# Performance work log

Hardware: AMD Instinct MI355X
Metric: run time of the kernel (lower is better)

## Reference

```python
import jax, jax.numpy as jnp
import numpy as np

B, S, E = 1, 2048, 4096
HQ, HKV = 32, 8
D = E // HQ          # 128
RATIO = HQ // HKV    # 4
CACHE = 1024
T = CACHE + S        # 3072


def setup_inputs() -> dict:
    key = jax.random.key(0)
    ks = jax.random.split(key, 8)
    sc = lambda fan_in: 1.0 / np.sqrt(fan_in)
    x = jax.random.normal(ks[0], (B, S, E), dtype=jnp.float32)
    w_q = jax.random.normal(ks[1], (E, E), dtype=jnp.float32) * sc(E)
    w_k = jax.random.normal(ks[2], (E, HKV * D), dtype=jnp.float32) * sc(E)
    w_v = jax.random.normal(ks[3], (E, HKV * D), dtype=jnp.float32) * sc(E)
    w_o = jax.random.normal(ks[4], (E, E), dtype=jnp.float32) * sc(E)
    k_cache = jax.random.normal(ks[5], (B, HKV, CACHE, D), dtype=jnp.float32)
    v_cache = jax.random.normal(ks[6], (B, HKV, CACHE, D), dtype=jnp.float32)
    # causal additive mask with cache offset: query i may attend key j iff j <= i + CACHE
    q_pos = jnp.arange(S)[:, None] + CACHE
    k_pos = jnp.arange(T)[None, :]
    attention_mask = jnp.where(k_pos <= q_pos, 0.0, -1e9).astype(jnp.float32)
    return {"x": x, "w_q": w_q, "w_k": w_k, "w_v": w_v, "w_o": w_o,
            "k_cache": k_cache, "v_cache": v_cache, "attention_mask": attention_mask}


def reference(x, w_q, w_k, w_v, w_o, k_cache, v_cache, attention_mask):
    # Projections, split into heads: [B, H, S, D]
    Q = (x @ w_q).reshape(B, S, HQ, D).transpose(0, 2, 1, 3)
    K_new = (x @ w_k).reshape(B, S, HKV, D).transpose(0, 2, 1, 3)
    V_new = (x @ w_v).reshape(B, S, HKV, D).transpose(0, 2, 1, 3)
    # KV-cache concat along time
    K = jnp.concatenate([k_cache, K_new], axis=2)  # [B, HKV, T, D]
    V = jnp.concatenate([v_cache, V_new], axis=2)
    # GQA grouping as in source: (head group) with group = HKV
    Qg = Q.reshape(B, RATIO, HKV, S, D)            # [B, h, g, S, D]
    scores = jnp.einsum('bhgsd,bgtd->bhgst', Qg, K) / jnp.sqrt(jnp.asarray(D, x.dtype))
    scores = scores + attention_mask               # broadcast [S, T]
    att = jax.nn.softmax(scores, axis=-1)
    res = jnp.einsum('bhgst,bgtd->bhgsd', att, V)  # [B, h, g, S, D]
    # '... head group s dhead -> ... s (head group dhead)'
    res = res.transpose(0, 3, 1, 2, 4).reshape(B, S, E)
    out = res @ w_o
    return (out, (K, V))
```

## Files before the change

kernel.cpp:

```cpp
#include <hip/hip_runtime.h>

typedef unsigned short u16;
typedef unsigned int u32;
typedef __attribute__((ext_vector_type(8))) short short8;
typedef __attribute__((ext_vector_type(4))) float f32x4;

#define S_LEN 2048
#define E_DIM 4096
#define NHQ 32
#define NHKV 8
#define HD 128
#define CACHE_LEN 1024
#define T_LEN 3072
#define KV_ELEMS ((size_t)NHKV * T_LEN * HD)

__device__ __forceinline__ u16 f2bf(float f) {
  union { float f; u32 u; } v; v.f = f;
  u32 u = v.u;
  return (u16)((u + 0x7FFFu + ((u >> 16) & 1u)) >> 16);
}

__device__ __forceinline__ void gl_lds16(const void* g, void* l) {
  __builtin_amdgcn_global_load_lds(
      (const __attribute__((address_space(1))) unsigned int*)g,
      (__attribute__((address_space(3))) unsigned int*)l, 16, 0, 0);
}

__global__ __launch_bounds__(256) void cvt_x(const float* __restrict__ x,
                                             u16* __restrict__ xb) {
  int i = blockIdx.x * 256 + threadIdx.x;
  float4 v = ((const float4*)x)[i];
  uint2 o;
  o.x = (u32)f2bf(v.x) | ((u32)f2bf(v.y) << 16);
  o.y = (u32)f2bf(v.z) | ((u32)f2bf(v.w) << 16);
  ((uint2*)xb)[i] = o;
}

__global__ __launch_bounds__(256) void copy_caches(
    const float4* __restrict__ kc, const float4* __restrict__ vc,
    float4* __restrict__ Ko, float4* __restrict__ Vo,
    uint2* __restrict__ Kb) {
  int i = blockIdx.x * 256 + threadIdx.x;
  int h = i >> 15;
  size_t o = (size_t)i + ((size_t)h << 16);
  float4 v = kc[i];
  Ko[o] = v;
  uint2 b;
  b.x = (u32)f2bf(v.x) | ((u32)f2bf(v.y) << 16);
  b.y = (u32)f2bf(v.z) | ((u32)f2bf(v.w) << 16);
  Kb[o] = b;
  Vo[o] = vc[i];
}

__global__ __launch_bounds__(256) void cvt_vcT(const float* __restrict__ vc,
                                               u16* __restrict__ vbT) {
  __shared__ u16 t[64][68];
  const int tid = threadIdx.x;
  const int h = blockIdx.z;
  const int t0 = blockIdx.x << 6;
  const int d0 = blockIdx.y << 6;
  const float* in = vc + ((size_t)h * CACHE_LEN + t0) * HD + d0;
  const int rl = tid >> 4;
  const int c4 = (tid & 15) << 2;
#pragma unroll
  for (int i = 0; i < 4; ++i) {
    int rr = rl + (i << 4);
    float4 v = *(const float4*)&in[(size_t)rr * HD + c4];
    t[c4 + 0][rr] = f2bf(v.x);
    t[c4 + 1][rr] = f2bf(v.y);
    t[c4 + 2][rr] = f2bf(v.z);
    t[c4 + 3][rr] = f2bf(v.w);
  }
  __syncthreads();
  u16* outp = vbT + ((size_t)h * HD + d0) * T_LEN + t0;
#pragma unroll
  for (int p = 0; p < 2; ++p) {
    int idx = tid + (p << 8);
    int dr = idx >> 3;
    int ch = (idx & 7) << 3;
    u32 a0 = (u32)t[dr][ch + 0] | ((u32)t[dr][ch + 1] << 16);
    u32 a1 = (u32)t[dr][ch + 2] | ((u32)t[dr][ch + 3] << 16);
    u32 a2 = (u32)t[dr][ch + 4] | ((u32)t[dr][ch + 5] << 16);
    u32 a3 = (u32)t[dr][ch + 6] | ((u32)t[dr][ch + 7] << 16);
    uint4 o4; o4.x = a0; o4.y = a1; o4.z = a2; o4.w = a3;
    *(uint4*)&outp[(size_t)dr * T_LEN + ch] = o4;
  }
}

__global__ __launch_bounds__(256) void cvt_wt(const float* __restrict__ w,
                                              u16* __restrict__ wt,
                                              int K, int N) {
  __shared__ u16 t[64][68];
  const int tid = threadIdx.x;
  const int ntk = K >> 6;
  const int k0 = (blockIdx.x % ntk) << 6;
  const int n0 = (blockIdx.x / ntk) << 6;
  const int kl = tid >> 4;
  const int nl4 = (tid & 15) << 2;
#pragma unroll
  for (int i = 0; i < 4; ++i) {
    int kk = kl + (i << 4);
    float4 v = *(const float4*)&w[(size_t)(k0 + kk) * N + n0 + nl4];
    t[nl4 + 0][kk] = f2bf(v.x);
    t[nl4 + 1][kk] = f2bf(v.y);
    t[nl4 + 2][kk] = f2bf(v.z);
    t[nl4 + 3][kk] = f2bf(v.w);
  }
  __syncthreads();
  const int onl = tid >> 3;
  const int okc = (tid & 7) << 3;
#pragma unroll
  for (int p = 0; p < 2; ++p) {
    int nl = onl + (p << 5);
    u32 a0 = (u32)t[nl][okc + 0] | ((u32)t[nl][okc + 1] << 16);
    u32 a1 = (u32)t[nl][okc + 2] | ((u32)t[nl][okc + 3] << 16);
    u32 a2 = (u32)t[nl][okc + 4] | ((u32)t[nl][okc + 5] << 16);
    u32 a3 = (u32)t[nl][okc + 6] | ((u32)t[nl][okc + 7] << 16);
    uint4 o4; o4.x = a0; o4.y = a1; o4.z = a2; o4.w = a3;
    *(uint4*)&wt[(size_t)(n0 + nl) * K + k0 + okc] = o4;
  }
}

template<int MODE>
__global__ __launch_bounds__(256) void gemm2(
    const u16* __restrict__ A, const u16* __restrict__ Bt,
    int M, int N, int K,
    float* __restrict__ outF, u16* __restrict__ outB, u16* __restrict__ outB2) {
  __shared__ __align__(16) u16 Als[128 * 32];
  __shared__ __align__(16) u16 Bls[128 * 32];
  const int tid = threadIdx.x;
  const int lane = tid & 63;
  const int wave = tid >> 6;
  const int wr = wave >> 1, wc = wave & 1;
  const int l15 = lane & 15, l4 = lane >> 4;
  const int nbn = N >> 7;
  const int bm0 = (blockIdx.x / nbn) << 7;
  const int bn0 = (blockIdx.x % nbn) << 7;

  f32x4 acc[4][4];
#pragma unroll
  for (int i = 0; i < 4; ++i)
#pragma unroll
    for (int j = 0; j < 4; ++j) {
      acc[i][j][0] = 0.f; acc[i][j][1] = 0.f;
      acc[i][j][2] = 0.f; acc[i][j][3] = 0.f;
    }

  const u16* Abase = A + (size_t)bm0 * K;
  const u16* Bbase = Bt + (size_t)bn0 * K;
  const int c0 = tid, c1 = tid + 256;
  const int r0 = c0 >> 2, q0c = (c0 & 3) << 3;
  const int r1 = c1 >> 2, q1c = (c1 & 3) << 3;

  for (int k0 = 0; k0 < K; k0 += 32) {
    __syncthreads();
    gl_lds16(Abase + (size_t)r0 * K + k0 + q0c, &Als[c0 << 3]);
    gl_lds16(Bbase + (size_t)r0 * K + k0 + q0c, &Bls[c0 << 3]);
    gl_lds16(Abase + (size_t)r1 * K + k0 + q1c, &Als[c1 << 3]);
    gl_lds16(Bbase + (size_t)r1 * K + k0 + q1c, &Bls[c1 << 3]);
    __syncthreads();

    short8 af[4], bfr[4];
#pragma unroll
    for (int mi = 0; mi < 4; ++mi)
      af[mi] = *(const short8*)&Als[((wr << 6) + (mi << 4) + l15) * 32 + (l4 << 3)];
#pragma unroll
    for (int ni = 0; ni < 4; ++ni)
      bfr[ni] = *(const short8*)&Bls[((wc << 6) + (ni << 4) + l15) * 32 + (l4 << 3)];
#pragma unroll
    for (int mi = 0; mi < 4; ++mi)
#pragma unroll
      for (int ni = 0; ni < 4; ++ni)
        acc[mi][ni] = __builtin_amdgcn_mfma_f32_16x16x32_bf16(af[mi], bfr[ni],
                                                              acc[mi][ni], 0, 0, 0);
  }
#pragma unroll
  for (int mi = 0; mi < 4; ++mi) {
#pragma unroll
    for (int ni = 0; ni < 4; ++ni) {
#pragma unroll
      for (int r = 0; r < 4; ++r) {
        int row = bm0 + (wr << 6) + (mi << 4) + (l4 << 2) + r;
        int col = bn0 + (wc << 6) + (ni << 4) + l15;
        float v = acc[mi][ni][r];
        if (MODE == 0) {
          outB[(size_t)row * N + col] = f2bf(v);
        } else if (MODE == 1) {
          int hv = col >> 7;
          int d = col & 127;
          int h = hv & 7;
          if (hv < 8) {
            size_t idx = ((size_t)h * T_LEN + (CACHE_LEN + row)) * HD + d;
            outF[idx] = v;
            outB[idx] = f2bf(v);
          } else {
            size_t idxF = ((size_t)h * T_LEN + (CACHE_LEN + row)) * HD + d + KV_ELEMS;
            outF[idxF] = v;
            outB2[((size_t)h * HD + d) * T_LEN + (CACHE_LEN + row)] = f2bf(v);
          }
        } else {
          outF[(size_t)row * N + col] = v;
        }
      }
    }
  }
}

__global__ __launch_bounds__(256) void attn_fwd(
    const u16* __restrict__ Qb, const u16* __restrict__ Kb,
    const u16* __restrict__ VbT, u16* __restrict__ resB) {
  __shared__ __align__(16) u16 Kls[2][64 * 128];
  __shared__ __align__(16) u16 Vls[2][128 * 64];
  __shared__ __align__(16) u16 Pls[4][16][72];
  const int tid = threadIdx.x;
  const int lane = tid & 63;
  const int wave = tid >> 6;
  const int l15 = lane & 15, l4 = lane >> 4;
  const int hq = blockIdx.y;
  const int kvh = hq & 7;
  const int bx = (hq & 1) ? (31 - (int)blockIdx.x) : (int)blockIdx.x;
  const int q0 = bx << 6;
  const int qw = q0 + (wave << 4);

  short8 aq[4];
  const u16* qrow = Qb + (size_t)(qw + l15) * E_DIM + hq * HD;
#pragma unroll
  for (int kd = 0; kd < 4; ++kd)
    aq[kd] = *(const short8*)(qrow + (kd << 5) + (l4 << 3));

  f32x4 accO[8];
  float mrow[4], lrow[4];
#pragma unroll
  for (int nd = 0; nd < 8; ++nd) {
    accO[nd][0] = 0.f; accO[nd][1] = 0.f; accO[nd][2] = 0.f; accO[nd][3] = 0.f;
  }
#pragma unroll
  for (int r = 0; r < 4; ++r) { mrow[r] = -1e30f; lrow[r] = 0.f; }

  const u16* Kh = Kb + (size_t)kvh * T_LEN * HD;
  const u16* VTh = VbT + (size_t)kvh * (size_t)HD * T_LEN;
  const int nt = bx + 17;

#define STAGE_TILE(T0, BUF)                                                   \
  {                                                                           \
    _Pragma("unroll")                                                         \
    for (int s = 0; s < 4; ++s) {                                             \
      int tr = (wave << 4) + (s << 2) + (lane >> 4);                          \
      int jd = (lane & 15) ^ (tr & 7);                                        \
      gl_lds16(Kh + (size_t)((T0) + tr) * HD + (jd << 3),                     \
               &Kls[BUF][((wave << 2) + s) << 9]);                            \
      int dr = (wave << 5) + (s << 3) + (lane >> 3);                          \
      int tj = (lane & 7) ^ (dr & 7);                                         \
      gl_lds16(VTh + (size_t)dr * T_LEN + (T0) + (tj << 3),                   \
               &Vls[BUF][((wave << 2) + s) << 9]);                            \
    }                                                                         \
  }

  STAGE_TILE(0, 0);
  __syncthreads();

  const float scale = 0.08838834764831845f;
  const int xr = (l15 & 7) << 3;

  for (int it = 0; it < nt; ++it) {
    const int cur = it & 1;
    const int t0 = it << 6;
    if (it + 1 < nt) STAGE_TILE(t0 + 64, cur ^ 1);

    const u16* Kc = &Kls[cur][0];
    const u16* Vc = &Vls[cur][0];

    float p[4][4];
#pragma unroll
    for (int ct = 0; ct < 4; ++ct) {
      f32x4 sc;
      sc[0] = 0.f; sc[1] = 0.f; sc[2] = 0.f; sc[3] = 0.f;
#pragma unroll
      for (int kd = 0; kd < 4; ++kd) {
        short8 bk = *(const short8*)&Kc[((ct << 4) + l15) * 128 +
                                        (((kd << 5) + (l4 << 3)) ^ xr)];
        sc = __builtin_amdgcn_mfma_f32_16x16x32_bf16(aq[kd], bk, sc, 0, 0, 0);
      }
#pragma unroll
      for (int r = 0; r < 4; ++r) p[ct][r] = sc[r] * scale;
    }

    const bool need_mask = (t0 + 63) > (q0 + CACHE_LEN);
    if (need_mask) {
#pragma unroll
      for (int ct = 0; ct < 4; ++ct)
#pragma unroll
        for (int r = 0; r < 4; ++r) {
          int qq = qw + (l4 << 2) + r + CACHE_LEN;
          if (t0 + (ct << 4) + l15 > qq) p[ct][r] = -1e30f;
        }
    }

#pragma unroll
    for (int r = 0; r < 4; ++r) {
      float mx = fmaxf(fmaxf(p[0][r], p[1][r]), fmaxf(p[2][r], p[3][r]));
      mx = fmaxf(mx, __shfl_xor(mx, 1));
      mx = fmaxf(mx, __shfl_xor(mx, 2));
      mx = fmaxf(mx, __shfl_xor(mx, 4));
      mx = fmaxf(mx, __shfl_xor(mx, 8));
      float mn = fmaxf(mrow[r], mx);
      float corr = __expf(mrow[r] - mn);
      mrow[r] = mn;
      float rs = 0.f;
#pragma unroll
      for (int ct = 0; ct < 4; ++ct) {
        p[ct][r] = __expf(p[ct][r] - mn);
        rs += p[ct][r];
      }
      rs += __shfl_xor(rs, 1);
      rs += __shfl_xor(rs, 2);
      rs += __shfl_xor(rs, 4);
      rs += __shfl_xor(rs, 8);
      lrow[r] = lrow[r] * corr + rs;
#pragma unroll
      for (int nd = 0; nd < 8; ++nd) accO[nd][r] *= corr;
    }

#pragma unroll
    for (int ct = 0; ct < 4; ++ct)
#pragma unroll
      for (int r = 0; r < 4; ++r)
        Pls[wave][(l4 << 2) + r][(ct << 4) + l15] = f2bf(p[ct][r]);
    short8 pa0 = *(const short8*)&Pls[wave][l15][l4 << 3];
    short8 pa1 = *(const short8*)&Pls[wave][l15][32 + (l4 << 3)];

#pragma unroll
    for (int nd = 0; nd < 8; ++nd) {
      short8 bv0 = *(const short8*)&Vc[((nd << 4) + l15) * 64 + ((l4 << 3) ^ xr)];
      accO[nd] = __builtin_amdgcn_mfma_f32_16x16x32_bf16(pa0, bv0, accO[nd], 0, 0, 0);
      short8 bv1 = *(const short8*)&Vc[((nd << 4) + l15) * 64 + ((32 + (l4 << 3)) ^ xr)];
      accO[nd] = __builtin_amdgcn_mfma_f32_16x16x32_bf16(pa1, bv1, accO[nd], 0, 0, 0);
    }
    __syncthreads();
  }
#undef STAGE_TILE

#pragma unroll
  for (int nd = 0; nd < 8; ++nd) {
#pragma unroll
    for (int r = 0; r < 4; ++r) {
      float v = accO[nd][r] / lrow[r];
      int q = qw + (l4 << 2) + r;
      int d = (nd << 4) + l15;
      resB[(size_t)q * E_DIM + hq * HD + d] = f2bf(v);
    }
  }
}

extern "C" void kernel_launch(void* const* d_in, const int* in_sizes, int n_in,
                              void* d_out, int out_size, void* d_ws, size_t ws_size,
                              hipStream_t stream) {
  const float* x = (const float*)d_in[0];
  const float* w_q = (const float*)d_in[1];
  const float* w_k = (const float*)d_in[2];
  const float* w_v = (const float*)d_in[3];
  const float* w_o = (const float*)d_in[4];
  const float* k_cache = (const float*)d_in[5];
  const float* v_cache = (const float*)d_in[6];

  float* out = (float*)d_out;
  float* Kout = out + (size_t)S_LEN * E_DIM;

  char* ws = (char*)d_ws;
  const size_t MB = 1024 * 1024;
  u16* xb   = (u16*)(ws);
  u16* resB = (u16*)(ws);
  u16* Qb   = (u16*)(ws + 16 * MB);
  u16* Kb   = (u16*)(ws + 32 * MB);
  u16* VbT  = (u16*)(ws + 38 * MB);
  u16* wkvt = (u16*)(ws + 48 * MB);
  u16* wbig = (u16*)(ws + 64 * MB);

  cvt_x<<<dim3(8192), dim3(256), 0, stream>>>(x, xb);
  copy_caches<<<dim3(1024), dim3(256), 0, stream>>>(
      (const float4*)k_cache, (const float4*)v_cache,
      (float4*)Kout, (float4*)(Kout + KV_ELEMS), (uint2*)Kb);
  cvt_vcT<<<dim3(16, 2, 8), dim3(256), 0, stream>>>(v_cache, VbT);
  cvt_wt<<<dim3(1024), dim3(256), 0, stream>>>(w_k, wkvt, E_DIM, NHKV * HD);
  cvt_wt<<<dim3(1024), dim3(256), 0, stream>>>(w_v, wkvt + (size_t)1024 * E_DIM, E_DIM, NHKV * HD);
  cvt_wt<<<dim3(4096), dim3(256), 0, stream>>>(w_q, wbig, E_DIM, E_DIM);
  gemm2<1><<<dim3(16 * 16), dim3(256), 0, stream>>>(xb, wkvt, S_LEN, 2048, E_DIM, Kout, Kb, VbT);
  gemm2<0><<<dim3(16 * 32), dim3(256), 0, stream>>>(xb, wbig, S_LEN, E_DIM, E_DIM, nullptr, Qb, nullptr);
  cvt_wt<<<dim3(4096), dim3(256), 0, stream>>>(w_o, wbig, E_DIM, E_DIM);
  attn_fwd<<<dim3(32, 32), dim3(256), 0, stream>>>(Qb, Kb, VbT, resB);
  gemm2<2><<<dim3(16 * 32), dim3(256), 0, stream>>>(resB, wbig, S_LEN, E_DIM, E_DIM, out, nullptr, nullptr);
}
```

Measured before the change: 793.2 us.

## Enlarge attention query tile to 256 rows with two row groups per wave

The attention kernel now launches 512-thread blocks that each cover 256 query rows, with every wave processing two 16-row groups. Each staged K/V tile is therefore reused by four times as many queries, cutting global and LDS staging traffic per query. It also adds a lazy softmax rescale that only corrects the accumulators when the row max grows by more than 8, and uses a reciprocal in the epilogue. The costs are higher register pressure, coarser causal tiles that do some extra masked work, and a different block ordering that drops the previous load-balancing flip. The lazy rescale may also change numerics slightly.

```diff
diff --git a/kernel.cpp b/kernel.cpp
--- a/kernel.cpp
+++ b/kernel.cpp
@@ -206,57 +206,69 @@
   }
 }
 
-__global__ __launch_bounds__(256) void attn_fwd(
+__global__ __launch_bounds__(512, 2) void attn_fwd(
     const u16* __restrict__ Qb, const u16* __restrict__ Kb,
     const u16* __restrict__ VbT, u16* __restrict__ resB) {
   __shared__ __align__(16) u16 Kls[2][64 * 128];
   __shared__ __align__(16) u16 Vls[2][128 * 64];
-  __shared__ __align__(16) u16 Pls[4][16][72];
+  __shared__ __align__(16) u16 Pls[8][16][72];
   const int tid = threadIdx.x;
   const int lane = tid & 63;
   const int wave = tid >> 6;
   const int l15 = lane & 15, l4 = lane >> 4;
-  const int hq = blockIdx.y;
+  const int bid = blockIdx.x;
+  const int hq = bid & 31;
+  const int bx = bid >> 5;
   const int kvh = hq & 7;
-  const int bx = (hq & 1) ? (31 - (int)blockIdx.x) : (int)blockIdx.x;
-  const int q0 = bx << 6;
-  const int qw = q0 + (wave << 4);
-
-  short8 aq[4];
-  const u16* qrow = Qb + (size_t)(qw + l15) * E_DIM + hq * HD;
-#pragma unroll
-  for (int kd = 0; kd < 4; ++kd)
-    aq[kd] = *(const short8*)(qrow + (kd << 5) + (l4 << 3));
-
-  f32x4 accO[8];
-  float mrow[4], lrow[4];
-#pragma unroll
-  for (int nd = 0; nd < 8; ++nd) {
-    accO[nd][0] = 0.f; accO[nd][1] = 0.f; accO[nd][2] = 0.f; accO[nd][3] = 0.f;
-  }
-#pragma unroll
-  for (int r = 0; r < 4; ++r) { mrow[r] = -1e30f; lrow[r] = 0.f; }
+  const int q0 = bx << 8;
+  const int qw = q0 + (wave << 5);
+
+  short8 aq[2][4];
+#pragma unroll
+  for (int rg = 0; rg < 2; ++rg) {
+    const u16* qrow = Qb + (size_t)(qw + (rg << 4) + l15) * E_DIM + hq * HD;
+#pragma unroll
+    for (int kd = 0; kd < 4; ++kd)
+      aq[rg][kd] = *(const short8*)(qrow + (kd << 5) + (l4 << 3));
+  }
+
+  f32x4 accO[2][8];
+  float mrow[2][4], lrow[2][4];
+#pragma unroll
+  for (int rg = 0; rg < 2; ++rg) {
+#pragma unroll
+    for (int nd = 0; nd < 8; ++nd) {
+      accO[rg][nd][0] = 0.f; accO[rg][nd][1] = 0.f;
+      accO[rg][nd][2] = 0.f; accO[rg][nd][3] = 0.f;
+    }
+#pragma unroll
+    for (int r = 0; r < 4; ++r) { mrow[rg][r] = -1e30f; lrow[rg][r] = 0.f; }
+  }
 
   const u16* Kh = Kb + (size_t)kvh * T_LEN * HD;
   const u16* VTh = VbT + (size_t)kvh * (size_t)HD * T_LEN;
-  const int nt = bx + 17;
-
-#define STAGE_TILE(T0, BUF)                                                   \
-  {                                                                           \
-    _Pragma("unroll")                                                         \
-    for (int s = 0; s < 4; ++s) {                                             \
-      int tr = (wave << 4) + (s << 2) + (lane >> 4);                          \
-      int jd = (lane & 15) ^ (tr & 7);                                        \
-      gl_lds16(Kh + (size_t)((T0) + tr) * HD + (jd << 3),                     \
-               &Kls[BUF][((wave << 2) + s) << 9]);                            \
-      int dr = (wave << 5) + (s << 3) + (lane >> 3);                          \
-      int tj = (lane & 7) ^ (dr & 7);                                         \
-      gl_lds16(VTh + (size_t)dr * T_LEN + (T0) + (tj << 3),                   \
-               &Vls[BUF][((wave << 2) + s) << 9]);                            \
-    }                                                                         \
-  }
-
-  STAGE_TILE(0, 0);
+  const int nt = (bx << 2) + 20;
+
+  const int trk = (wave << 3) + (lane >> 4);
+  const int jd0 = (lane & 15) ^ (trk & 7);
+  const int jd1 = (lane & 15) ^ ((trk + 4) & 7);
+  const u16* kp0 = Kh + (size_t)trk * HD + (jd0 << 3);
+  const u16* kp1 = Kh + (size_t)(trk + 4) * HD + (jd1 << 3);
+  const int drv = (wave << 4) + (lane >> 3);
+  const int tj0 = (lane & 7) ^ (drv & 7);
+  const u16* vp0 = VTh + (size_t)drv * T_LEN + (tj0 << 3);
+  const u16* vp1 = VTh + (size_t)(drv + 8) * T_LEN + (tj0 << 3);
+
+#define STAGE(BUF)                                             \
+  {                                                            \
+    gl_lds16(kp0, &Kls[BUF][((wave << 1) + 0) << 9]);          \
+    gl_lds16(kp1, &Kls[BUF][((wave << 1) + 1) << 9]);          \
+    gl_lds16(vp0, &Vls[BUF][((wave << 1) + 0) << 9]);          \
+    gl_lds16(vp1, &Vls[BUF][((wave << 1) + 1) << 9]);          \
+    kp0 += 64 * HD; kp1 += 64 * HD; vp0 += 64; vp1 += 64;      \
+  }
+
+  STAGE(0);
   __syncthreads();
 
   const float scale = 0.08838834764831845f;
@@ -265,89 +277,112 @@
   for (int it = 0; it < nt; ++it) {
     const int cur = it & 1;
     const int t0 = it << 6;
-    if (it + 1 < nt) STAGE_TILE(t0 + 64, cur ^ 1);
+    if (it + 1 < nt) STAGE(cur ^ 1);
 
     const u16* Kc = &Kls[cur][0];
     const u16* Vc = &Vls[cur][0];
 
-    float p[4][4];
-#pragma unroll
-    for (int ct = 0; ct < 4; ++ct) {
-      f32x4 sc;
-      sc[0] = 0.f; sc[1] = 0.f; sc[2] = 0.f; sc[3] = 0.f;
-#pragma unroll
-      for (int kd = 0; kd < 4; ++kd) {
-        short8 bk = *(const short8*)&Kc[((ct << 4) + l15) * 128 +
-                                        (((kd << 5) + (l4 << 3)) ^ xr)];
-        sc = __builtin_amdgcn_mfma_f32_16x16x32_bf16(aq[kd], bk, sc, 0, 0, 0);
-      }
-#pragma unroll
-      for (int r = 0; r < 4; ++r) p[ct][r] = sc[r] * scale;
-    }
-
-    const bool need_mask = (t0 + 63) > (q0 + CACHE_LEN);
-    if (need_mask) {
+#pragma unroll
+    for (int rg = 0; rg < 2; ++rg) {
+      const int qrg = qw + (rg << 4);
+      float p[4][4];
+#pragma unroll
+      for (int ct = 0; ct < 4; ++ct) {
+        f32x4 sc;
+        sc[0] = 0.f; sc[1] = 0.f; sc[2] = 0.f; sc[3] = 0.f;
+#pragma unroll
+        for (int kd = 0; kd < 4; ++kd) {
+          short8 bk = *(const short8*)&Kc[((ct << 4) + l15) * 128 +
+                                          (((kd << 5) + (l4 << 3)) ^ xr)];
+          sc = __builtin_amdgcn_mfma_f32_16x16x32_bf16(aq[rg][kd], bk, sc, 0, 0, 0);
+        }
+#pragma unroll
+        for (int r = 0; r < 4; ++r) p[ct][r] = sc[r] * scale;
+      }
+
+      if ((t0 + 63) > (qrg + CACHE_LEN)) {
+#pragma unroll
+        for (int ct = 0; ct < 4; ++ct)
+#pragma unroll
+          for (int r = 0; r < 4; ++r) {
+            int qq = qrg + (l4 << 2) + r + CACHE_LEN;
+            if (t0 + (ct << 4) + l15 > qq) p[ct][r] = -1e30f;
+          }
+      }
+
+      float mx[4];
+#pragma unroll
+      for (int r = 0; r < 4; ++r) {
+        float m = fmaxf(fmaxf(p[0][r], p[1][r]), fmaxf(p[2][r], p[3][r]));
+        m = fmaxf(m, __shfl_xor(m, 1));
+        m = fmaxf(m, __shfl_xor(m, 2));
+        m = fmaxf(m, __shfl_xor(m, 4));
+        m = fmaxf(m, __shfl_xor(m, 8));
+        mx[r] = m;
+      }
+      bool grow = false;
+#pragma unroll
+      for (int r = 0; r < 4; ++r) grow = grow || (mx[r] > mrow[rg][r] + 8.f);
+      if (__any(grow)) {
+#pragma unroll
+        for (int r = 0; r < 4; ++r) {
+          float mn = fmaxf(mrow[rg][r], mx[r]);
+          float corr = __expf(mrow[rg][r] - mn);
+          mrow[rg][r] = mn;
+          lrow[rg][r] *= corr;
+#pragma unroll
+          for (int nd = 0; nd < 8; ++nd) accO[rg][nd][r] *= corr;
+        }
+      }
+#pragma unroll
+      for (int r = 0; r < 4; ++r) {
+        float rs = 0.f;
+#pragma unroll
+        for (int ct = 0; ct < 4; ++ct) {
+          p[ct][r] = __expf(p[ct][r] - mrow[rg][r]);
+          rs += p[ct][r];
+        }
+        rs += __shfl_xor(rs, 1);
+        rs += __shfl_xor(rs, 2);
+        rs += __shfl_xor(rs, 4);
+        rs += __shfl_xor(rs, 8);
+        lrow[rg][r] += rs;
+      }
+
 #pragma unroll
       for (int ct = 0; ct < 4; ++ct)
 #pragma unroll
-        for (int r = 0; r < 4; ++r) {
-          int qq = qw + (l4 << 2) + r + CACHE_LEN;
-          if (t0 + (ct << 4) + l15 > qq) p[ct][r] = -1e30f;
-        }
-    }
-
-#pragma unroll
-    for (int r = 0; r < 4; ++r) {
-      float mx = fmaxf(fmaxf(p[0][r], p[1][r]), fmaxf(p[2][r], p[3][r]));
-      mx = fmaxf(mx, __shfl_xor(mx, 1));
-      mx = fmaxf(mx, __shfl_xor(mx, 2));
-      mx = fmaxf(mx, __shfl_xor(mx, 4));
-      mx = fmaxf(mx, __shfl_xor(mx, 8));
-      float mn = fmaxf(mrow[r], mx);
-      float corr = __expf(mrow[r] - mn);
-      mrow[r] = mn;
-      float rs = 0.f;
-#pragma unroll
-      for (int ct = 0; ct < 4; ++ct) {
-        p[ct][r] = __expf(p[ct][r] - mn);
-        rs += p[ct][r];
-      }
-      rs += __shfl_xor(rs, 1);
-      rs += __shfl_xor(rs, 2);
-      rs += __shfl_xor(rs, 4);
-      rs += __shfl_xor(rs, 8);
-      lrow[r] = lrow[r] * corr + rs;
-#pragma unroll
-      for (int nd = 0; nd < 8; ++nd) accO[nd][r] *= corr;
-    }
-
-#pragma unroll
-    for (int ct = 0; ct < 4; ++ct)
-#pragma unroll
-      for (int r = 0; r < 4; ++r)
-        Pls[wave][(l4 << 2) + r][(ct << 4) + l15] = f2bf(p[ct][r]);
-    short8 pa0 = *(const short8*)&Pls[wave][l15][l4 << 3];
-    short8 pa1 = *(const short8*)&Pls[wave][l15][32 + (l4 << 3)];
-
-#pragma unroll
-    for (int nd = 0; nd < 8; ++nd) {
-      short8 bv0 = *(const short8*)&Vc[((nd << 4) + l15) * 64 + ((l4 << 3) ^ xr)];
-      accO[nd] = __builtin_amdgcn_mfma_f32_16x16x32_bf16(pa0, bv0, accO[nd], 0, 0, 0);
-      short8 bv1 = *(const short8*)&Vc[((nd << 4) + l15) * 64 + ((32 + (l4 << 3)) ^ xr)];
-      accO[nd] = __builtin_amdgcn_mfma_f32_16x16x32_bf16(pa1, bv1, accO[nd], 0, 0, 0);
+        for (int r = 0; r < 4; ++r)
+          Pls[wave][(l4 << 2) + r][(ct << 4) + l15] = f2bf(p[ct][r]);
+      short8 pa0 = *(const short8*)&Pls[wave][l15][l4 << 3];
+      short8 pa1 = *(const short8*)&Pls[wave][l15][32 + (l4 << 3)];
+
+#pragma unroll
+      for (int nd = 0; nd < 8; ++nd) {
+        short8 bv0 = *(const short8*)&Vc[((nd << 4) + l15) * 64 + ((l4 << 3) ^ xr)];
+        accO[rg][nd] = __builtin_amdgcn_mfma_f32_16x16x32_bf16(pa0, bv0, accO[rg][nd], 0, 0, 0);
+        short8 bv1 = *(const short8*)&Vc[((nd << 4) + l15) * 64 + ((32 + (l4 << 3)) ^ xr)];
+        accO[rg][nd] = __builtin_amdgcn_mfma_f32_16x16x32_bf16(pa1, bv1, accO[rg][nd], 0, 0, 0);
+      }
     }
     __syncthreads();
   }
-#undef STAGE_TILE
-
-#pragma unroll
-  for (int nd = 0; nd < 8; ++nd) {
-#pragma unroll
-    for (int r = 0; r < 4; ++r) {
-      float v = accO[nd][r] / lrow[r];
-      int q = qw + (l4 << 2) + r;
-      int d = (nd << 4) + l15;
-      resB[(size_t)q * E_DIM + hq * HD + d] = f2bf(v);
+#undef STAGE
+
+#pragma unroll
+  for (int rg = 0; rg < 2; ++rg) {
+    float inv[4];
+#pragma unroll
+    for (int r = 0; r < 4; ++r) inv[r] = 1.0f / lrow[rg][r];
+#pragma unroll
+    for (int nd = 0; nd < 8; ++nd) {
+#pragma unroll
+      for (int r = 0; r < 4; ++r) {
+        float v = accO[rg][nd][r] * inv[r];
+        int q = qw + (rg << 4) + (l4 << 2) + r;
+        int d = (nd << 4) + l15;
+        resB[(size_t)q * E_DIM + hq * HD + d] = f2bf(v);
+      }
     }
   }
 }
@@ -387,6 +422,6 @@
   gemm2<1><<<dim3(16 * 16), dim3(256), 0, stream>>>(xb, wkvt, S_LEN, 2048, E_DIM, Kout, Kb, VbT);
   gemm2<0><<<dim3(16 * 32), dim3(256), 0, stream>>>(xb, wbig, S_LEN, E_DIM, E_DIM, nullptr, Qb, nullptr);
   cvt_wt<<<dim3(4096), dim3(256), 0, stream>>>(w_o, wbig, E_DIM, E_DIM);
-  attn_fwd<<<dim3(32, 32), dim3(256), 0, stream>>>(Qb, Kb, VbT, resB);
+  attn_fwd<<<dim3(256), dim3(512), 0, stream>>>(Qb, Kb, VbT, resB);
   gemm2<2><<<dim3(16 * 32), dim3(256), 0, stream>>>(resB, wbig, S_LEN, E_DIM, E_DIM, out, nullptr, nullptr);
 }
```

Result: faster. 754.8 us (-4.8%).
